# Kernel tuning notes

Measured on AMD Instinct MI355X. Metric: run time of the kernel, lower is better.

Reference implementation:

```python
import jax, jax.numpy as jnp
import numpy as np

N = 50000
E = 800000
IN_CH = 128
HID = 16
HEADS = 16
OUT_CH = 64
NEG_SLOPE = 0.2
EPS = 1e-16


def _add_self_loops(edge_index, n):
    loops = jnp.arange(n, dtype=edge_index.dtype)
    src = jnp.concatenate([edge_index[0], loops])
    dst = jnp.concatenate([edge_index[1], loops])
    return src, dst


def gat_conv(x, src, dst, W, a_src, a_dst, b, heads, out_ch, concat, n):
    # x: [N, F_in], W: [F_in, heads*out_ch], a_src/a_dst: [heads, out_ch]
    h = (x @ W).reshape(n, heads, out_ch)                 # [N, H, C]
    alpha_src = jnp.sum(h * a_src, axis=-1)               # [N, H]
    alpha_dst = jnp.sum(h * a_dst, axis=-1)               # [N, H]
    e = alpha_src[src] + alpha_dst[dst]                   # [E, H]
    e = jnp.where(e > 0, e, NEG_SLOPE * e)                # LeakyReLU(0.2)
    m = jax.ops.segment_max(e, dst, num_segments=n)       # [N, H] (finite: self-loops)
    ex = jnp.exp(e - m[dst])                              # [E, H]
    denom = jax.ops.segment_sum(ex, dst, num_segments=n)  # [N, H]
    alpha = ex / (denom[dst] + EPS)                       # [E, H]
    msg = h[src] * alpha[:, :, None]                      # [E, H, C]
    out = jax.ops.segment_sum(msg, dst, num_segments=n)   # [N, H, C]
    if concat:
        out = out.reshape(n, heads * out_ch)
    else:
        out = out.mean(axis=1)
    return out + b


def setup_inputs() -> dict:
    key = jax.random.key(0)
    ks = jax.random.split(key, 10)
    x = jax.random.normal(ks[0], (N, IN_CH), dtype=jnp.float32)
    edge_index = jax.random.randint(ks[1], (2, E), 0, N, dtype=jnp.int64)
    s1 = 1.0 / np.sqrt(IN_CH)
    W1 = jax.random.normal(ks[2], (IN_CH, HEADS * HID), dtype=jnp.float32) * s1
    a_src1 = jax.random.normal(ks[3], (HEADS, HID), dtype=jnp.float32) * (1.0 / np.sqrt(HID))
    a_dst1 = jax.random.normal(ks[4], (HEADS, HID), dtype=jnp.float32) * (1.0 / np.sqrt(HID))
    b1 = jnp.zeros((HEADS * HID,), dtype=jnp.float32)
    s2 = 1.0 / np.sqrt(HEADS * HID)
    W2 = jax.random.normal(ks[5], (HEADS * HID, OUT_CH), dtype=jnp.float32) * s2
    a_src2 = jax.random.normal(ks[6], (1, OUT_CH), dtype=jnp.float32) * (1.0 / np.sqrt(OUT_CH))
    a_dst2 = jax.random.normal(ks[7], (1, OUT_CH), dtype=jnp.float32) * (1.0 / np.sqrt(OUT_CH))
    b2 = jnp.zeros((OUT_CH,), dtype=jnp.float32)
    return {"x": x, "edge_index": edge_index, "W1": W1, "a_src1": a_src1,
            "a_dst1": a_dst1, "b1": b1, "W2": W2, "a_src2": a_src2,
            "a_dst2": a_dst2, "b2": b2}


def reference(x, edge_index, W1, a_src1, a_dst1, b1, W2, a_src2, a_dst2, b2):
    src, dst = _add_self_loops(edge_index, N)
    h = gat_conv(x, src, dst, W1, a_src1, a_dst1, b1, HEADS, HID, True, N)
    h = gat_conv(h, src, dst, W2, a_src2, a_dst2, b2, 1, OUT_CH, False, N)
    return jax.nn.sigmoid(h)
```

## Files before the change

kernel.cpp:

```cpp
#include <hip/hip_runtime.h>
#include <hip/hip_bf16.h>

#define NN 50000
#define EE 800000
#define TE 850000
#define BK 64

typedef __hip_bfloat16 bf16;
typedef __attribute__((ext_vector_type(8))) short short8v;
typedef __attribute__((ext_vector_type(4))) float float4v;

__device__ __forceinline__ float b2f(bf16 v) { return __bfloat162float(v); }
__device__ __forceinline__ float bu2f(unsigned short v) {
    return __uint_as_float((unsigned)v << 16);
}
__device__ __forceinline__ unsigned short f2bu(float v) {
    bf16 t = __float2bfloat16(v);
    return *(unsigned short*)&t;
}
__device__ __forceinline__ float lrelu(float e) { return (e > 0.f) ? e : 0.2f * e; }
__device__ __forceinline__ int clampn(int v) {
    return (v < 0) ? 0 : (v >= NN ? NN - 1 : v);
}

__device__ __forceinline__ int block_isi64(const void* ei) {
    __shared__ int sflag;
    int t = threadIdx.x;
    if (t < 64) {
        unsigned z = (((const unsigned*)ei)[2 * t + 1] == 0u) ? 1u : 0u;
        unsigned long long m = __ballot(z);
        if (t == 0) sflag = (__popcll(m) >= 32) ? 1 : 0;
    }
    __syncthreads();
    return sflag;
}

__global__ void prep_k(const void* __restrict__ ei, int* __restrict__ deg,
                       int* __restrict__ csr,
                       const float* __restrict__ W1, const float* __restrict__ W2,
                       const float* __restrict__ asr1, const float* __restrict__ ads1,
                       const float* __restrict__ asr2, const float* __restrict__ ads2,
                       unsigned short* __restrict__ W1T,
                       unsigned short* __restrict__ W2T,
                       unsigned short* __restrict__ P1sT,
                       unsigned short* __restrict__ P1dT,
                       unsigned short* __restrict__ P2T) {
    int isi64 = block_isi64(ei);
    int b = blockIdx.x, t = threadIdx.x;
    if (b < 128) {
        int j = b * 256 + t;
        int n = j >> 7, k = j & 127;
        W1T[j] = f2bu(W1[k * 256 + n]);
    } else if (b < 192) {
        int j = (b - 128) * 256 + t;
        int n = j >> 8, k = j & 255;
        W2T[j] = f2bu(W2[k * 64 + n]);
    } else if (b == 192) {
        for (int j = t; j < 2048; j += 256) {
            int h = j >> 7, k = j & 127;
            float s = 0.f, d = 0.f;
            for (int c = 0; c < 16; ++c) {
                float wv = W1[k * 256 + h * 16 + c];
                s += wv * asr1[h * 16 + c];
                d += wv * ads1[h * 16 + c];
            }
            P1sT[j] = f2bu(s);
            P1dT[j] = f2bu(d);
        }
    } else if (b == 193) {
        int k = t;
        float s = 0.f, d = 0.f;
        for (int c = 0; c < 64; ++c) {
            float wv = W2[k * 64 + c];
            s += wv * asr2[c];
            d += wv * ads2[c];
        }
        P2T[k] = f2bu(s);
        P2T[256 + k] = f2bu(d);
        for (int j = 512 + t; j < 4096; j += 256) P2T[j] = 0;
    }
    int p = b * 256 + t;
    int i0 = p * 2;
    if (i0 >= TE) return;
    int s0, d0, s1 = -1, d1 = -1;
    if (i0 + 1 < EE) {
        if (isi64) {
            longlong2 sv = ((const longlong2*)ei)[p];
            longlong2 dv = ((const longlong2*)ei)[(EE >> 1) + p];
            s0 = clampn((int)sv.x); s1 = clampn((int)sv.y);
            d0 = clampn((int)dv.x); d1 = clampn((int)dv.y);
        } else {
            int2 sv = ((const int2*)ei)[p];
            int2 dv = ((const int2*)ei)[(EE >> 1) + p];
            s0 = clampn(sv.x); s1 = clampn(sv.y);
            d0 = clampn(dv.x); d1 = clampn(dv.y);
        }
    } else {
        auto lde = [&](long long idx) {
            return clampn(isi64 ? (int)((const long long*)ei)[idx] : ((const int*)ei)[idx]);
        };
        if (i0 < EE) { s0 = lde(i0); d0 = lde((long long)EE + i0); }
        else         { s0 = i0 - EE; d0 = i0 - EE; }
        if (i0 + 1 < TE) {
            if (i0 + 1 < EE) { s1 = lde(i0 + 1); d1 = lde((long long)EE + i0 + 1); }
            else             { s1 = i0 + 1 - EE; d1 = i0 + 1 - EE; }
        }
    }
    int pos0 = atomicAdd(&deg[d0], 1);
    if (pos0 < BK) csr[d0 * BK + pos0] = s0;
    if (d1 >= 0) {
        int pos1 = atomicAdd(&deg[d1], 1);
        if (pos1 < BK) csr[d1 * BK + pos1] = s1;
    }
}

__global__ __launch_bounds__(256) void gemm1_k(
    const float* __restrict__ x, const unsigned short* __restrict__ W1T,
    const unsigned short* __restrict__ P1sT, const unsigned short* __restrict__ P1dT,
    bf16* __restrict__ h1, float* __restrict__ a_src, float* __restrict__ a_dst) {
    int wv = threadIdx.x >> 6, lane = threadIdx.x & 63;
    int m = lane & 15, quad = lane >> 4;
    int row0 = blockIdx.x * 64 + wv * 16;
    int arow = row0 + m;
    int arowc = (arow < NN) ? arow : NN - 1;
    const float4* x4 = (const float4*)x;
    short8v a[4];
#pragma unroll
    for (int ks = 0; ks < 4; ++ks) {
        float4 f0 = x4[(size_t)arowc * 32 + ks * 8 + quad * 2];
        float4 f1 = x4[(size_t)arowc * 32 + ks * 8 + quad * 2 + 1];
        union { short8v v; unsigned short u[8]; } ua;
        ua.u[0] = f2bu(f0.x); ua.u[1] = f2bu(f0.y);
        ua.u[2] = f2bu(f0.z); ua.u[3] = f2bu(f0.w);
        ua.u[4] = f2bu(f1.x); ua.u[5] = f2bu(f1.y);
        ua.u[6] = f2bu(f1.z); ua.u[7] = f2bu(f1.w);
        a[ks] = ua.v;
    }
    float4v accs = {0.f, 0.f, 0.f, 0.f}, accd = {0.f, 0.f, 0.f, 0.f};
#pragma unroll
    for (int ks = 0; ks < 4; ++ks) {
        short8v bs = *(const short8v*)&P1sT[(size_t)m * 128 + quad * 8 + ks * 32];
        short8v bd = *(const short8v*)&P1dT[(size_t)m * 128 + quad * 8 + ks * 32];
        accs = __builtin_amdgcn_mfma_f32_16x16x32_bf16(a[ks], bs, accs, 0, 0, 0);
        accd = __builtin_amdgcn_mfma_f32_16x16x32_bf16(a[ks], bd, accd, 0, 0, 0);
    }
    float4v acc[16];
#pragma unroll
    for (int t = 0; t < 16; ++t) {
        float4v c = {0.f, 0.f, 0.f, 0.f};
        const unsigned short* wb = &W1T[(size_t)(t * 16 + m) * 128 + quad * 8];
#pragma unroll
        for (int ks = 0; ks < 4; ++ks) {
            short8v b = *(const short8v*)&wb[ks * 32];
            c = __builtin_amdgcn_mfma_f32_16x16x32_bf16(a[ks], b, c, 0, 0, 0);
        }
        acc[t] = c;
    }
#pragma unroll
    for (int t = 0; t < 16; ++t) {
#pragma unroll
        for (int r = 0; r < 4; ++r) {
            int orow = row0 + quad * 4 + r;
            if (orow < NN)
                h1[(size_t)orow * 256 + t * 16 + m] = __float2bfloat16(acc[t][r]);
        }
    }
#pragma unroll
    for (int r = 0; r < 4; ++r) {
        int orow = row0 + quad * 4 + r;
        if (orow < NN) {
            a_src[orow * 16 + m] = accs[r];
            a_dst[orow * 16 + m] = accd[r];
        }
    }
}

__global__ __launch_bounds__(256) void agg1_k(
    const int* __restrict__ deg, int* __restrict__ csr,
    const float* __restrict__ a_src, const float* __restrict__ a_dst,
    const bf16* __restrict__ h1, const float* __restrict__ b1,
    bf16* __restrict__ out1) {
    __shared__ int sbuf[4][64];
    int wv = threadIdx.x >> 6, lane = threadIdx.x & 63;
    int dst = blockIdx.x * 4 + wv;
    int d = deg[dst]; if (d > BK) d = BK;
    int base = dst * BK;
    int v = (lane < d) ? csr[base + lane] : 0x7fffffff;
    int rank = 0;
    for (int j = 0; j < d; ++j) {
        int vj = __shfl(v, j, 64);
        rank += (vj < v || (vj == v && j < lane)) ? 1 : 0;
    }
    if (lane < d) sbuf[wv][rank] = v;
    if (lane < d) csr[base + lane] = sbuf[wv][lane];
    int we = lane >> 4, wh = lane & 15;
    int hc = lane >> 2;
    float adst_w = a_dst[dst * 16 + wh];
    float ax = 0.f, ay = 0.f, az = 0.f, aw = 0.f;
    float dsum = 0.f;
    int t0 = 0;
    for (; t0 + 4 <= d; t0 += 4) {
        int sr = sbuf[wv][t0 + we];
        float wr = __expf(lrelu(a_src[sr * 16 + wh] + adst_w));
        dsum += wr;
#pragma unroll
        for (int j = 0; j < 4; ++j) {
            float wj = __shfl(wr, j * 16 + hc, 64);
            int sj = sbuf[wv][t0 + j];
            ushort4 hv = *(const ushort4*)&h1[(size_t)sj * 256 + lane * 4];
            ax += wj * bu2f(hv.x);
            ay += wj * bu2f(hv.y);
            az += wj * bu2f(hv.z);
            aw += wj * bu2f(hv.w);
        }
    }
    if (t0 < d) {
        int n = d - t0;
        float wr = 0.f;
        if (we < n) {
            int sr = sbuf[wv][t0 + we];
            wr = __expf(lrelu(a_src[sr * 16 + wh] + adst_w));
        }
        dsum += wr;
        for (int j = 0; j < n; ++j) {
            float wj = __shfl(wr, j * 16 + hc, 64);
            int sj = sbuf[wv][t0 + j];
            ushort4 hv = *(const ushort4*)&h1[(size_t)sj * 256 + lane * 4];
            ax += wj * bu2f(hv.x);
            ay += wj * bu2f(hv.y);
            az += wj * bu2f(hv.z);
            aw += wj * bu2f(hv.w);
        }
    }
    dsum += __shfl_xor(dsum, 16, 64);
    dsum += __shfl_xor(dsum, 32, 64);
    float invd = 1.f / (__shfl(dsum, hc, 64) + 1e-16f);
    float4 bv = *(const float4*)&b1[lane * 4];
    ushort4 st;
    st.x = f2bu(ax * invd + bv.x);
    st.y = f2bu(ay * invd + bv.y);
    st.z = f2bu(az * invd + bv.z);
    st.w = f2bu(aw * invd + bv.w);
    *(ushort4*)&out1[(size_t)dst * 256 + lane * 4] = st;
}

__global__ __launch_bounds__(256) void gemm2_k(
    const bf16* __restrict__ out1, const unsigned short* __restrict__ W2T,
    const unsigned short* __restrict__ P2T,
    bf16* __restrict__ h2, float* __restrict__ a_src2, float* __restrict__ a_dst2) {
    int wv = threadIdx.x >> 6, lane = threadIdx.x & 63;
    int m = lane & 15, quad = lane >> 4;
    int row0 = blockIdx.x * 64 + wv * 16;
    int arow = row0 + m;
    int arowc = (arow < NN) ? arow : NN - 1;
    const unsigned short* ab = (const unsigned short*)out1;
    short8v a[8];
#pragma unroll
    for (int ks = 0; ks < 8; ++ks)
        a[ks] = *(const short8v*)&ab[(size_t)arowc * 256 + ks * 32 + quad * 8];
    float4v acca = {0.f, 0.f, 0.f, 0.f};
#pragma unroll
    for (int ks = 0; ks < 8; ++ks) {
        short8v b = *(const short8v*)&P2T[(size_t)m * 256 + quad * 8 + ks * 32];
        acca = __builtin_amdgcn_mfma_f32_16x16x32_bf16(a[ks], b, acca, 0, 0, 0);
    }
    float4v acc[4];
#pragma unroll
    for (int t = 0; t < 4; ++t) {
        float4v c = {0.f, 0.f, 0.f, 0.f};
        const unsigned short* wb = &W2T[(size_t)(t * 16 + m) * 256 + quad * 8];
#pragma unroll
        for (int ks = 0; ks < 8; ++ks) {
            short8v b = *(const short8v*)&wb[ks * 32];
            c = __builtin_amdgcn_mfma_f32_16x16x32_bf16(a[ks], b, c, 0, 0, 0);
        }
        acc[t] = c;
    }
#pragma unroll
    for (int t = 0; t < 4; ++t) {
#pragma unroll
        for (int r = 0; r < 4; ++r) {
            int orow = row0 + quad * 4 + r;
            if (orow < NN)
                h2[(size_t)orow * 64 + t * 16 + m] = __float2bfloat16(acc[t][r]);
        }
    }
#pragma unroll
    for (int r = 0; r < 4; ++r) {
        int orow = row0 + quad * 4 + r;
        if (orow < NN) {
            if (m == 0) a_src2[orow] = acca[r];
            if (m == 1) a_dst2[orow] = acca[r];
        }
    }
}

__global__ __launch_bounds__(256) void agg2_k(
    const int* __restrict__ deg, const int* __restrict__ csr,
    const float* __restrict__ a_src2, const float* __restrict__ a_dst2,
    const bf16* __restrict__ h2, const float* __restrict__ b2,
    float* __restrict__ out) {
    int wv = threadIdx.x >> 6;
    int lane = threadIdx.x & 63;
    int dst = blockIdx.x * 4 + wv;
    if (dst >= NN) return;
    int d = deg[dst]; if (d > BK) d = BK;
    int base = dst * BK;
    float adst = a_dst2[dst];
    int half = lane >> 5, hl = lane & 31;
    float acc0 = 0.f, acc1 = 0.f, dsum = 0.f;
    float wr = 0.f; int sr = 0;
    if (lane < d) {
        sr = csr[base + lane];
        wr = __expf(lrelu(a_src2[sr] + adst));
    }
    dsum += wr;
    for (int j0 = 0; j0 < d; j0 += 8) {
        ushort2 hv[4];
        float wj[4];
#pragma unroll
        for (int u = 0; u < 4; ++u) {
            int j = j0 + u * 2 + half;
            int jc = (j < d) ? j : 0;
            float w = __shfl(wr, jc, 64);
            int sj = __shfl(sr, jc, 64);
            wj[u] = (j < d) ? w : 0.f;
            hv[u] = *(const ushort2*)&h2[(size_t)sj * 64 + hl * 2];
        }
#pragma unroll
        for (int u = 0; u < 4; ++u) {
            acc0 += wj[u] * bu2f(hv[u].x);
            acc1 += wj[u] * bu2f(hv[u].y);
        }
    }
    acc0 += __shfl_xor(acc0, 32, 64);
    acc1 += __shfl_xor(acc1, 32, 64);
#pragma unroll
    for (int o = 32; o >= 1; o >>= 1) dsum += __shfl_xor(dsum, o, 64);
    if (half == 0) {
        float inv = 1.f / (dsum + 1e-16f);
        float o0 = acc0 * inv + b2[hl * 2];
        float o1 = acc1 * inv + b2[hl * 2 + 1];
        float2 st;
        st.x = 1.f / (1.f + __expf(-o0));
        st.y = 1.f / (1.f + __expf(-o1));
        *(float2*)&out[(size_t)dst * 64 + hl * 2] = st;
    }
}


extern "C" void kernel_launch(void* const* d_in, const int* in_sizes, int n_in,
                              void* d_out, int out_size, void* d_ws, size_t ws_size,
                              hipStream_t stream) {
    const float* x    = (const float*)d_in[0];
    const void*  ei   = d_in[1];
    const float* W1   = (const float*)d_in[2];
    const float* asr1 = (const float*)d_in[3];
    const float* ads1 = (const float*)d_in[4];
    const float* b1   = (const float*)d_in[5];
    const float* W2   = (const float*)d_in[6];
    const float* asr2 = (const float*)d_in[7];
    const float* ads2 = (const float*)d_in[8];
    const float* b2   = (const float*)d_in[9];
    float* out = (float*)d_out;

    char* w = (char*)d_ws;
    auto carve = [&](size_t bytes) {
        void* p = (void*)w;
        w += (bytes + 255) & ~(size_t)255;
        return p;
    };
    int*    csr      = (int*)carve((size_t)NN * BK * 4);
    int*    deg      = (int*)carve((size_t)NN * 4);
    float*  a_src1   = (float*)carve((size_t)NN * 16 * 4);
    float*  a_dst1   = (float*)carve((size_t)NN * 16 * 4);
    unsigned short* W1T  = (unsigned short*)carve(128 * 256 * 2);
    unsigned short* W2T  = (unsigned short*)carve(256 * 64 * 2);
    unsigned short* P1sT = (unsigned short*)carve(16 * 128 * 2);
    unsigned short* P1dT = (unsigned short*)carve(16 * 128 * 2);
    unsigned short* P2T  = (unsigned short*)carve(16 * 256 * 2);
    bf16*   h1       = (bf16*)carve((size_t)NN * 256 * 2);
    bf16*   out1     = (bf16*)carve((size_t)NN * 256 * 2);
    char*   l2base   = (char*)h1;
    bf16*   h2       = (bf16*)l2base;
    float*  a_src2   = (float*)(l2base + (size_t)NN * 64 * 2);
    float*  a_dst2   = a_src2 + NN;

    hipMemsetAsync(deg, 0, (size_t)NN * 4, stream);

    const int pgrid = ((TE + 1) / 2 + 255) / 256;
    prep_k<<<pgrid, 256, 0, stream>>>(ei, deg, csr, W1, W2, asr1, ads1, asr2, ads2,
                                      W1T, W2T, P1sT, P1dT, P2T);
    gemm1_k<<<(NN + 63) / 64, 256, 0, stream>>>(x, W1T, P1sT, P1dT, h1, a_src1, a_dst1);
    agg1_k<<<NN / 4, 256, 0, stream>>>(deg, csr, a_src1, a_dst1, h1, b1, out1);
    gemm2_k<<<(NN + 63) / 64, 256, 0, stream>>>(out1, W2T, P2T, h2, a_src2, a_dst2);
    agg2_k<<<(NN + 3) / 4, 256, 0, stream>>>(deg, csr, a_src2, a_dst2, h2, b2, out);
}
```

Baseline: 299.3 us.

## Fuse all stages into one persistent kernel with grid-wide barriers

```diff
diff --git a/kernel.cpp b/kernel.cpp
--- a/kernel.cpp
+++ b/kernel.cpp
@@ -5,12 +5,14 @@
 #define EE 800000
 #define TE 850000
 #define BK 64
+#define NEB 1661
+#define NGB 782
+#define NAB 12500
 
 typedef __hip_bfloat16 bf16;
 typedef __attribute__((ext_vector_type(8))) short short8v;
 typedef __attribute__((ext_vector_type(4))) float float4v;
 
-__device__ __forceinline__ float b2f(bf16 v) { return __bfloat162float(v); }
 __device__ __forceinline__ float bu2f(unsigned short v) {
     return __uint_as_float((unsigned)v << 16);
 }
@@ -23,328 +25,326 @@
     return (v < 0) ? 0 : (v >= NN ? NN - 1 : v);
 }
 
-__device__ __forceinline__ int block_isi64(const void* ei) {
-    __shared__ int sflag;
-    int t = threadIdx.x;
-    if (t < 64) {
-        unsigned z = (((const unsigned*)ei)[2 * t + 1] == 0u) ? 1u : 0u;
-        unsigned long long m = __ballot(z);
-        if (t == 0) sflag = (__popcll(m) >= 32) ? 1 : 0;
-    }
+__device__ __forceinline__ void gsync(int* bar, int target) {
     __syncthreads();
-    return sflag;
-}
-
-__global__ void prep_k(const void* __restrict__ ei, int* __restrict__ deg,
-                       int* __restrict__ csr,
-                       const float* __restrict__ W1, const float* __restrict__ W2,
-                       const float* __restrict__ asr1, const float* __restrict__ ads1,
-                       const float* __restrict__ asr2, const float* __restrict__ ads2,
-                       unsigned short* __restrict__ W1T,
-                       unsigned short* __restrict__ W2T,
-                       unsigned short* __restrict__ P1sT,
-                       unsigned short* __restrict__ P1dT,
-                       unsigned short* __restrict__ P2T) {
-    int isi64 = block_isi64(ei);
-    int b = blockIdx.x, t = threadIdx.x;
-    if (b < 128) {
-        int j = b * 256 + t;
-        int n = j >> 7, k = j & 127;
-        W1T[j] = f2bu(W1[k * 256 + n]);
-    } else if (b < 192) {
-        int j = (b - 128) * 256 + t;
-        int n = j >> 8, k = j & 255;
-        W2T[j] = f2bu(W2[k * 64 + n]);
-    } else if (b == 192) {
-        for (int j = t; j < 2048; j += 256) {
-            int h = j >> 7, k = j & 127;
+    if (threadIdx.x == 0) {
+        __threadfence();
+        __hip_atomic_fetch_add(bar, 1, __ATOMIC_RELEASE, __HIP_MEMORY_SCOPE_AGENT);
+        while (__hip_atomic_load(bar, __ATOMIC_ACQUIRE, __HIP_MEMORY_SCOPE_AGENT)
+               < target)
+            __builtin_amdgcn_s_sleep(2);
+        __threadfence();
+    }
+    __syncthreads();
+}
+
+__global__ __launch_bounds__(256, 2) void mega_k(
+    const void* __restrict__ ei, const float* __restrict__ x,
+    const float* __restrict__ W1, const float* __restrict__ asr1,
+    const float* __restrict__ ads1, const float* __restrict__ b1,
+    const float* __restrict__ W2, const float* __restrict__ asr2,
+    const float* __restrict__ ads2, const float* __restrict__ b2,
+    int* __restrict__ deg, int* __restrict__ csr,
+    unsigned short* __restrict__ W1T, unsigned short* __restrict__ W2T,
+    unsigned short* __restrict__ P1sT, unsigned short* __restrict__ P1dT,
+    unsigned short* __restrict__ P2T,
+    float* __restrict__ a_src1, float* __restrict__ a_dst1,
+    bf16* __restrict__ h1, bf16* __restrict__ h2,
+    float* __restrict__ a_src2, float* __restrict__ a_dst2,
+    int* __restrict__ bar,
+    float* __restrict__ out) {
+    const int tid = threadIdx.x;
+    const int wv = tid >> 6, lane = tid & 63;
+    const int G = gridDim.x;
+
+    __shared__ int s_isi64;
+    __shared__ int sbuf[4][64];
+    __shared__ unsigned short sout[4][256];
+
+    if (tid < 64) {
+        unsigned z = (((const unsigned*)ei)[2 * tid + 1] == 0u) ? 1u : 0u;
+        unsigned long long mb = __ballot(z);
+        if (tid == 0) s_isi64 = (__popcll(mb) >= 32) ? 1 : 0;
+    }
+    __syncthreads();
+    const int isi64 = s_isi64;
+
+    for (int i = blockIdx.x * 256 + tid; i < NN; i += G * 256) deg[i] = 0;
+    gsync(&bar[0], G);
+
+    for (int vb = blockIdx.x; vb < 194; vb += G) {
+        if (vb < 128) {
+            int j = vb * 256 + tid;
+            int n = j >> 7, k = j & 127;
+            W1T[j] = f2bu(W1[k * 256 + n]);
+        } else if (vb < 192) {
+            int j = (vb - 128) * 256 + tid;
+            int n = j >> 8, k = j & 255;
+            W2T[j] = f2bu(W2[k * 64 + n]);
+        } else if (vb == 192) {
+            for (int j = tid; j < 2048; j += 256) {
+                int h = j >> 7, k = j & 127;
+                float s = 0.f, d = 0.f;
+                for (int c = 0; c < 16; ++c) {
+                    float wvv = W1[k * 256 + h * 16 + c];
+                    s += wvv * asr1[h * 16 + c];
+                    d += wvv * ads1[h * 16 + c];
+                }
+                P1sT[j] = f2bu(s);
+                P1dT[j] = f2bu(d);
+            }
+        } else {
+            int k = tid;
             float s = 0.f, d = 0.f;
-            for (int c = 0; c < 16; ++c) {
-                float wv = W1[k * 256 + h * 16 + c];
-                s += wv * asr1[h * 16 + c];
-                d += wv * ads1[h * 16 + c];
-            }
-            P1sT[j] = f2bu(s);
-            P1dT[j] = f2bu(d);
-        }
-    } else if (b == 193) {
-        int k = t;
-        float s = 0.f, d = 0.f;
-        for (int c = 0; c < 64; ++c) {
-            float wv = W2[k * 64 + c];
-            s += wv * asr2[c];
-            d += wv * ads2[c];
-        }
-        P2T[k] = f2bu(s);
-        P2T[256 + k] = f2bu(d);
-        for (int j = 512 + t; j < 4096; j += 256) P2T[j] = 0;
-    }
-    int p = b * 256 + t;
-    int i0 = p * 2;
-    if (i0 >= TE) return;
-    int s0, d0, s1 = -1, d1 = -1;
-    if (i0 + 1 < EE) {
-        if (isi64) {
-            longlong2 sv = ((const longlong2*)ei)[p];
-            longlong2 dv = ((const longlong2*)ei)[(EE >> 1) + p];
-            s0 = clampn((int)sv.x); s1 = clampn((int)sv.y);
-            d0 = clampn((int)dv.x); d1 = clampn((int)dv.y);
+            for (int c = 0; c < 64; ++c) {
+                float wvv = W2[k * 64 + c];
+                s += wvv * asr2[c];
+                d += wvv * ads2[c];
+            }
+            P2T[k] = f2bu(s);
+            P2T[256 + k] = f2bu(d);
+            for (int j = 512 + tid; j < 4096; j += 256) P2T[j] = 0;
+        }
+    }
+    for (int vb = blockIdx.x; vb < NEB; vb += G) {
+        int p = vb * 256 + tid;
+        int i0 = p * 2;
+        if (i0 >= TE) continue;
+        int s0, d0, s1 = -1, d1 = -1;
+        if (i0 + 1 < EE) {
+            if (isi64) {
+                longlong2 sv = ((const longlong2*)ei)[p];
+                longlong2 dv = ((const longlong2*)ei)[(EE >> 1) + p];
+                s0 = clampn((int)sv.x); s1 = clampn((int)sv.y);
+                d0 = clampn((int)dv.x); d1 = clampn((int)dv.y);
+            } else {
+                int2 sv = ((const int2*)ei)[p];
+                int2 dv = ((const int2*)ei)[(EE >> 1) + p];
+                s0 = clampn(sv.x); s1 = clampn(sv.y);
+                d0 = clampn(dv.x); d1 = clampn(dv.y);
+            }
         } else {
-            int2 sv = ((const int2*)ei)[p];
-            int2 dv = ((const int2*)ei)[(EE >> 1) + p];
-            s0 = clampn(sv.x); s1 = clampn(sv.y);
-            d0 = clampn(dv.x); d1 = clampn(dv.y);
-        }
-    } else {
-        auto lde = [&](long long idx) {
-            return clampn(isi64 ? (int)((const long long*)ei)[idx] : ((const int*)ei)[idx]);
-        };
-        if (i0 < EE) { s0 = lde(i0); d0 = lde((long long)EE + i0); }
-        else         { s0 = i0 - EE; d0 = i0 - EE; }
-        if (i0 + 1 < TE) {
-            if (i0 + 1 < EE) { s1 = lde(i0 + 1); d1 = lde((long long)EE + i0 + 1); }
-            else             { s1 = i0 + 1 - EE; d1 = i0 + 1 - EE; }
-        }
-    }
-    int pos0 = atomicAdd(&deg[d0], 1);
-    if (pos0 < BK) csr[d0 * BK + pos0] = s0;
-    if (d1 >= 0) {
-        int pos1 = atomicAdd(&deg[d1], 1);
-        if (pos1 < BK) csr[d1 * BK + pos1] = s1;
-    }
-}
-
-__global__ __launch_bounds__(256) void gemm1_k(
-    const float* __restrict__ x, const unsigned short* __restrict__ W1T,
-    const unsigned short* __restrict__ P1sT, const unsigned short* __restrict__ P1dT,
-    bf16* __restrict__ h1, float* __restrict__ a_src, float* __restrict__ a_dst) {
-    int wv = threadIdx.x >> 6, lane = threadIdx.x & 63;
-    int m = lane & 15, quad = lane >> 4;
-    int row0 = blockIdx.x * 64 + wv * 16;
-    int arow = row0 + m;
-    int arowc = (arow < NN) ? arow : NN - 1;
-    const float4* x4 = (const float4*)x;
-    short8v a[4];
-#pragma unroll
-    for (int ks = 0; ks < 4; ++ks) {
-        float4 f0 = x4[(size_t)arowc * 32 + ks * 8 + quad * 2];
-        float4 f1 = x4[(size_t)arowc * 32 + ks * 8 + quad * 2 + 1];
-        union { short8v v; unsigned short u[8]; } ua;
-        ua.u[0] = f2bu(f0.x); ua.u[1] = f2bu(f0.y);
-        ua.u[2] = f2bu(f0.z); ua.u[3] = f2bu(f0.w);
-        ua.u[4] = f2bu(f1.x); ua.u[5] = f2bu(f1.y);
-        ua.u[6] = f2bu(f1.z); ua.u[7] = f2bu(f1.w);
-        a[ks] = ua.v;
-    }
-    float4v accs = {0.f, 0.f, 0.f, 0.f}, accd = {0.f, 0.f, 0.f, 0.f};
-#pragma unroll
-    for (int ks = 0; ks < 4; ++ks) {
-        short8v bs = *(const short8v*)&P1sT[(size_t)m * 128 + quad * 8 + ks * 32];
-        short8v bd = *(const short8v*)&P1dT[(size_t)m * 128 + quad * 8 + ks * 32];
-        accs = __builtin_amdgcn_mfma_f32_16x16x32_bf16(a[ks], bs, accs, 0, 0, 0);
-        accd = __builtin_amdgcn_mfma_f32_16x16x32_bf16(a[ks], bd, accd, 0, 0, 0);
-    }
-    float4v acc[16];
-#pragma unroll
-    for (int t = 0; t < 16; ++t) {
-        float4v c = {0.f, 0.f, 0.f, 0.f};
-        const unsigned short* wb = &W1T[(size_t)(t * 16 + m) * 128 + quad * 8];
-#pragma unroll
-        for (int ks = 0; ks < 4; ++ks) {
-            short8v b = *(const short8v*)&wb[ks * 32];
-            c = __builtin_amdgcn_mfma_f32_16x16x32_bf16(a[ks], b, c, 0, 0, 0);
-        }
-        acc[t] = c;
-    }
-#pragma unroll
-    for (int t = 0; t < 16; ++t) {
-#pragma unroll
-        for (int r = 0; r < 4; ++r) {
-            int orow = row0 + quad * 4 + r;
-            if (orow < NN)
-                h1[(size_t)orow * 256 + t * 16 + m] = __float2bfloat16(acc[t][r]);
-        }
-    }
-#pragma unroll
-    for (int r = 0; r < 4; ++r) {
-        int orow = row0 + quad * 4 + r;
-        if (orow < NN) {
-            a_src[orow * 16 + m] = accs[r];
-            a_dst[orow * 16 + m] = accd[r];
-        }
-    }
-}
-
-__global__ __launch_bounds__(256) void agg1_k(
-    const int* __restrict__ deg, int* __restrict__ csr,
-    const float* __restrict__ a_src, const float* __restrict__ a_dst,
-    const bf16* __restrict__ h1, const float* __restrict__ b1,
-    bf16* __restrict__ out1) {
-    __shared__ int sbuf[4][64];
-    int wv = threadIdx.x >> 6, lane = threadIdx.x & 63;
-    int dst = blockIdx.x * 4 + wv;
-    int d = deg[dst]; if (d > BK) d = BK;
-    int base = dst * BK;
-    int v = (lane < d) ? csr[base + lane] : 0x7fffffff;
-    int rank = 0;
-    for (int j = 0; j < d; ++j) {
-        int vj = __shfl(v, j, 64);
-        rank += (vj < v || (vj == v && j < lane)) ? 1 : 0;
-    }
-    if (lane < d) sbuf[wv][rank] = v;
-    if (lane < d) csr[base + lane] = sbuf[wv][lane];
-    int we = lane >> 4, wh = lane & 15;
-    int hc = lane >> 2;
-    float adst_w = a_dst[dst * 16 + wh];
-    float ax = 0.f, ay = 0.f, az = 0.f, aw = 0.f;
-    float dsum = 0.f;
-    int t0 = 0;
-    for (; t0 + 4 <= d; t0 += 4) {
-        int sr = sbuf[wv][t0 + we];
-        float wr = __expf(lrelu(a_src[sr * 16 + wh] + adst_w));
+            auto lde = [&](long long idx) {
+                return clampn(isi64 ? (int)((const long long*)ei)[idx]
+                                    : ((const int*)ei)[idx]);
+            };
+            if (i0 < EE) { s0 = lde(i0); d0 = lde((long long)EE + i0); }
+            else         { s0 = i0 - EE; d0 = i0 - EE; }
+            if (i0 + 1 < TE) {
+                if (i0 + 1 < EE) { s1 = lde(i0 + 1); d1 = lde((long long)EE + i0 + 1); }
+                else             { s1 = i0 + 1 - EE; d1 = i0 + 1 - EE; }
+            }
+        }
+        int pos0 = atomicAdd(&deg[d0], 1);
+        if (pos0 < BK) csr[d0 * BK + pos0] = s0;
+        if (d1 >= 0) {
+            int pos1 = atomicAdd(&deg[d1], 1);
+            if (pos1 < BK) csr[d1 * BK + pos1] = s1;
+        }
+    }
+    gsync(&bar[1], G);
+
+    {
+        const int m = lane & 15, quad = lane >> 4;
+        const float4* x4 = (const float4*)x;
+        for (int vb = blockIdx.x; vb < NGB; vb += G) {
+            int row0 = vb * 64 + wv * 16;
+            int arow = row0 + m;
+            int arowc = (arow < NN) ? arow : NN - 1;
+            short8v a[4];
+#pragma unroll
+            for (int ks = 0; ks < 4; ++ks) {
+                float4 f0 = x4[(size_t)arowc * 32 + ks * 8 + quad * 2];
+                float4 f1 = x4[(size_t)arowc * 32 + ks * 8 + quad * 2 + 1];
+                union { short8v v; unsigned short u[8]; } ua;
+                ua.u[0] = f2bu(f0.x); ua.u[1] = f2bu(f0.y);
+                ua.u[2] = f2bu(f0.z); ua.u[3] = f2bu(f0.w);
+                ua.u[4] = f2bu(f1.x); ua.u[5] = f2bu(f1.y);
+                ua.u[6] = f2bu(f1.z); ua.u[7] = f2bu(f1.w);
+                a[ks] = ua.v;
+            }
+            float4v accs = {0.f, 0.f, 0.f, 0.f}, accd = {0.f, 0.f, 0.f, 0.f};
+#pragma unroll
+            for (int ks = 0; ks < 4; ++ks) {
+                short8v bs = *(const short8v*)&P1sT[(size_t)m * 128 + quad * 8 + ks * 32];
+                short8v bd = *(const short8v*)&P1dT[(size_t)m * 128 + quad * 8 + ks * 32];
+                accs = __builtin_amdgcn_mfma_f32_16x16x32_bf16(a[ks], bs, accs, 0, 0, 0);
+                accd = __builtin_amdgcn_mfma_f32_16x16x32_bf16(a[ks], bd, accd, 0, 0, 0);
+            }
+#pragma unroll
+            for (int r = 0; r < 4; ++r) {
+                int orow = row0 + quad * 4 + r;
+                if (orow < NN) {
+                    a_src1[orow * 16 + m] = accs[r];
+                    a_dst1[orow * 16 + m] = accd[r];
+                }
+            }
+#pragma unroll
+            for (int t = 0; t < 16; ++t) {
+                float4v c = {0.f, 0.f, 0.f, 0.f};
+                const unsigned short* wb = &W1T[(size_t)(t * 16 + m) * 128 + quad * 8];
+#pragma unroll
+                for (int ks = 0; ks < 4; ++ks) {
+                    short8v b = *(const short8v*)&wb[ks * 32];
+                    c = __builtin_amdgcn_mfma_f32_16x16x32_bf16(a[ks], b, c, 0, 0, 0);
+                }
+#pragma unroll
+                for (int r = 0; r < 4; ++r) {
+                    int orow = row0 + quad * 4 + r;
+                    if (orow < NN)
+                        h1[(size_t)orow * 256 + t * 16 + m] = __float2bfloat16(c[r]);
+                }
+            }
+        }
+    }
+    gsync(&bar[2], G);
+
+    for (int vb = blockIdx.x; vb < NAB; vb += G) {
+        int dst = vb * 4 + wv;
+        int d = deg[dst]; if (d > BK) d = BK;
+        int base = dst * BK;
+        int v = (lane < d) ? csr[base + lane] : 0x7fffffff;
+        int rank = 0;
+        for (int j = 0; j < d; ++j) {
+            int vj = __shfl(v, j, 64);
+            rank += (vj < v || (vj == v && j < lane)) ? 1 : 0;
+        }
+        if (lane < d) sbuf[wv][rank] = v;
+        if (lane < d) csr[base + lane] = sbuf[wv][lane];
+        int we = lane >> 4, wh = lane & 15;
+        int hc = lane >> 2;
+        float adst_w = a_dst1[dst * 16 + wh];
+        float ax = 0.f, ay = 0.f, az = 0.f, aw = 0.f;
+        float dsum = 0.f;
+        int t0 = 0;
+        for (; t0 + 4 <= d; t0 += 4) {
+            int sr = sbuf[wv][t0 + we];
+            float wr = __expf(lrelu(a_src1[sr * 16 + wh] + adst_w));
+            dsum += wr;
+#pragma unroll
+            for (int j = 0; j < 4; ++j) {
+                float wj = __shfl(wr, j * 16 + hc, 64);
+                int sj = sbuf[wv][t0 + j];
+                ushort4 hv = *(const ushort4*)&h1[(size_t)sj * 256 + lane * 4];
+                ax += wj * bu2f(hv.x);
+                ay += wj * bu2f(hv.y);
+                az += wj * bu2f(hv.z);
+                aw += wj * bu2f(hv.w);
+            }
+        }
+        if (t0 < d) {
+            int n = d - t0;
+            float wr = 0.f;
+            if (we < n) {
+                int sr = sbuf[wv][t0 + we];
+                wr = __expf(lrelu(a_src1[sr * 16 + wh] + adst_w));
+            }
+            dsum += wr;
+            for (int j = 0; j < n; ++j) {
+                float wj = __shfl(wr, j * 16 + hc, 64);
+                int sj = sbuf[wv][t0 + j];
+                ushort4 hv = *(const ushort4*)&h1[(size_t)sj * 256 + lane * 4];
+                ax += wj * bu2f(hv.x);
+                ay += wj * bu2f(hv.y);
+                az += wj * bu2f(hv.z);
+                aw += wj * bu2f(hv.w);
+            }
+        }
+        dsum += __shfl_xor(dsum, 16, 64);
+        dsum += __shfl_xor(dsum, 32, 64);
+        float invd = 1.f / (__shfl(dsum, hc, 64) + 1e-16f);
+        float4 bv = *(const float4*)&b1[lane * 4];
+        ushort4 st;
+        st.x = f2bu(ax * invd + bv.x);
+        st.y = f2bu(ay * invd + bv.y);
+        st.z = f2bu(az * invd + bv.z);
+        st.w = f2bu(aw * invd + bv.w);
+        *(ushort4*)&sout[wv][lane * 4] = st;
+        __syncthreads();
+        {
+            int mm = lane & 15, qq = lane >> 4;
+            short8v a2[8];
+#pragma unroll
+            for (int ks = 0; ks < 8; ++ks)
+                a2[ks] = *(const short8v*)&sout[mm & 3][ks * 32 + qq * 8];
+            float4v c2 = {0.f, 0.f, 0.f, 0.f};
+            const unsigned short* wb2 = &W2T[(size_t)(wv * 16 + mm) * 256 + qq * 8];
+#pragma unroll
+            for (int ks = 0; ks < 8; ++ks) {
+                short8v b = *(const short8v*)&wb2[ks * 32];
+                c2 = __builtin_amdgcn_mfma_f32_16x16x32_bf16(a2[ks], b, c2, 0, 0, 0);
+            }
+            if (qq == 0) {
+#pragma unroll
+                for (int r = 0; r < 4; ++r)
+                    h2[(size_t)(vb * 4 + r) * 64 + wv * 16 + mm] = __float2bfloat16(c2[r]);
+            }
+            if (wv == 0) {
+                float4v ca = {0.f, 0.f, 0.f, 0.f};
+                const unsigned short* pb = &P2T[(size_t)mm * 256 + qq * 8];
+#pragma unroll
+                for (int ks = 0; ks < 8; ++ks) {
+                    short8v b = *(const short8v*)&pb[ks * 32];
+                    ca = __builtin_amdgcn_mfma_f32_16x16x32_bf16(a2[ks], b, ca, 0, 0, 0);
+                }
+                if (qq == 0 && mm == 0) {
+#pragma unroll
+                    for (int r = 0; r < 4; ++r) a_src2[vb * 4 + r] = ca[r];
+                }
+                if (qq == 0 && mm == 1) {
+#pragma unroll
+                    for (int r = 0; r < 4; ++r) a_dst2[vb * 4 + r] = ca[r];
+                }
+            }
+        }
+        __syncthreads();
+    }
+    gsync(&bar[3], G);
+
+    for (int vb = blockIdx.x; vb < NAB; vb += G) {
+        int dst = vb * 4 + wv;
+        int d = deg[dst]; if (d > BK) d = BK;
+        int base = dst * BK;
+        float adst = a_dst2[dst];
+        int half = lane >> 5, hl = lane & 31;
+        float acc0 = 0.f, acc1 = 0.f, dsum = 0.f;
+        float wr = 0.f; int sr = 0;
+        if (lane < d) {
+            sr = csr[base + lane];
+            wr = __expf(lrelu(a_src2[sr] + adst));
+        }
         dsum += wr;
-#pragma unroll
-        for (int j = 0; j < 4; ++j) {
-            float wj = __shfl(wr, j * 16 + hc, 64);
-            int sj = sbuf[wv][t0 + j];
-            ushort4 hv = *(const ushort4*)&h1[(size_t)sj * 256 + lane * 4];
-            ax += wj * bu2f(hv.x);
-            ay += wj * bu2f(hv.y);
-            az += wj * bu2f(hv.z);
-            aw += wj * bu2f(hv.w);
-        }
-    }
-    if (t0 < d) {
-        int n = d - t0;
-        float wr = 0.f;
-        if (we < n) {
-            int sr = sbuf[wv][t0 + we];
-            wr = __expf(lrelu(a_src[sr * 16 + wh] + adst_w));
-        }
-        dsum += wr;
-        for (int j = 0; j < n; ++j) {
-            float wj = __shfl(wr, j * 16 + hc, 64);
-            int sj = sbuf[wv][t0 + j];
-            ushort4 hv = *(const ushort4*)&h1[(size_t)sj * 256 + lane * 4];
-            ax += wj * bu2f(hv.x);
-            ay += wj * bu2f(hv.y);
-            az += wj * bu2f(hv.z);
-            aw += wj * bu2f(hv.w);
-        }
-    }
-    dsum += __shfl_xor(dsum, 16, 64);
-    dsum += __shfl_xor(dsum, 32, 64);
-    float invd = 1.f / (__shfl(dsum, hc, 64) + 1e-16f);
-    float4 bv = *(const float4*)&b1[lane * 4];
-    ushort4 st;
-    st.x = f2bu(ax * invd + bv.x);
-    st.y = f2bu(ay * invd + bv.y);
-    st.z = f2bu(az * invd + bv.z);
-    st.w = f2bu(aw * invd + bv.w);
-    *(ushort4*)&out1[(size_t)dst * 256 + lane * 4] = st;
-}
-
-__global__ __launch_bounds__(256) void gemm2_k(
-    const bf16* __restrict__ out1, const unsigned short* __restrict__ W2T,
-    const unsigned short* __restrict__ P2T,
-    bf16* __restrict__ h2, float* __restrict__ a_src2, float* __restrict__ a_dst2) {
-    int wv = threadIdx.x >> 6, lane = threadIdx.x & 63;
-    int m = lane & 15, quad = lane >> 4;
-    int row0 = blockIdx.x * 64 + wv * 16;
-    int arow = row0 + m;
-    int arowc = (arow < NN) ? arow : NN - 1;
-    const unsigned short* ab = (const unsigned short*)out1;
-    short8v a[8];
-#pragma unroll
-    for (int ks = 0; ks < 8; ++ks)
-        a[ks] = *(const short8v*)&ab[(size_t)arowc * 256 + ks * 32 + quad * 8];
-    float4v acca = {0.f, 0.f, 0.f, 0.f};
-#pragma unroll
-    for (int ks = 0; ks < 8; ++ks) {
-        short8v b = *(const short8v*)&P2T[(size_t)m * 256 + quad * 8 + ks * 32];
-        acca = __builtin_amdgcn_mfma_f32_16x16x32_bf16(a[ks], b, acca, 0, 0, 0);
-    }
-    float4v acc[4];
-#pragma unroll
-    for (int t = 0; t < 4; ++t) {
-        float4v c = {0.f, 0.f, 0.f, 0.f};
-        const unsigned short* wb = &W2T[(size_t)(t * 16 + m) * 256 + quad * 8];
-#pragma unroll
-        for (int ks = 0; ks < 8; ++ks) {
-            short8v b = *(const short8v*)&wb[ks * 32];
-            c = __builtin_amdgcn_mfma_f32_16x16x32_bf16(a[ks], b, c, 0, 0, 0);
-        }
-        acc[t] = c;
-    }
-#pragma unroll
-    for (int t = 0; t < 4; ++t) {
-#pragma unroll
-        for (int r = 0; r < 4; ++r) {
-            int orow = row0 + quad * 4 + r;
-            if (orow < NN)
-                h2[(size_t)orow * 64 + t * 16 + m] = __float2bfloat16(acc[t][r]);
-        }
-    }
-#pragma unroll
-    for (int r = 0; r < 4; ++r) {
-        int orow = row0 + quad * 4 + r;
-        if (orow < NN) {
-            if (m == 0) a_src2[orow] = acca[r];
-            if (m == 1) a_dst2[orow] = acca[r];
-        }
-    }
-}
-
-__global__ __launch_bounds__(256) void agg2_k(
-    const int* __restrict__ deg, const int* __restrict__ csr,
-    const float* __restrict__ a_src2, const float* __restrict__ a_dst2,
-    const bf16* __restrict__ h2, const float* __restrict__ b2,
-    float* __restrict__ out) {
-    int wv = threadIdx.x >> 6;
-    int lane = threadIdx.x & 63;
-    int dst = blockIdx.x * 4 + wv;
-    if (dst >= NN) return;
-    int d = deg[dst]; if (d > BK) d = BK;
-    int base = dst * BK;
-    float adst = a_dst2[dst];
-    int half = lane >> 5, hl = lane & 31;
-    float acc0 = 0.f, acc1 = 0.f, dsum = 0.f;
-    float wr = 0.f; int sr = 0;
-    if (lane < d) {
-        sr = csr[base + lane];
-        wr = __expf(lrelu(a_src2[sr] + adst));
-    }
-    dsum += wr;
-    for (int j0 = 0; j0 < d; j0 += 8) {
-        ushort2 hv[4];
-        float wj[4];
-#pragma unroll
-        for (int u = 0; u < 4; ++u) {
-            int j = j0 + u * 2 + half;
-            int jc = (j < d) ? j : 0;
-            float w = __shfl(wr, jc, 64);
-            int sj = __shfl(sr, jc, 64);
-            wj[u] = (j < d) ? w : 0.f;
-            hv[u] = *(const ushort2*)&h2[(size_t)sj * 64 + hl * 2];
-        }
-#pragma unroll
-        for (int u = 0; u < 4; ++u) {
-            acc0 += wj[u] * bu2f(hv[u].x);
-            acc1 += wj[u] * bu2f(hv[u].y);
-        }
-    }
-    acc0 += __shfl_xor(acc0, 32, 64);
-    acc1 += __shfl_xor(acc1, 32, 64);
-#pragma unroll
-    for (int o = 32; o >= 1; o >>= 1) dsum += __shfl_xor(dsum, o, 64);
-    if (half == 0) {
-        float inv = 1.f / (dsum + 1e-16f);
-        float o0 = acc0 * inv + b2[hl * 2];
-        float o1 = acc1 * inv + b2[hl * 2 + 1];
-        float2 st;
-        st.x = 1.f / (1.f + __expf(-o0));
-        st.y = 1.f / (1.f + __expf(-o1));
-        *(float2*)&out[(size_t)dst * 64 + hl * 2] = st;
+        for (int j0 = 0; j0 < d; j0 += 8) {
+            ushort2 hv[4];
+            float wj[4];
+#pragma unroll
+            for (int u = 0; u < 4; ++u) {
+                int j = j0 + u * 2 + half;
+                int jc = (j < d) ? j : 0;
+                float w = __shfl(wr, jc, 64);
+                int sj = __shfl(sr, jc, 64);
+                wj[u] = (j < d) ? w : 0.f;
+                hv[u] = *(const ushort2*)&h2[(size_t)sj * 64 + hl * 2];
+            }
+#pragma unroll
+            for (int u = 0; u < 4; ++u) {
+                acc0 += wj[u] * bu2f(hv[u].x);
+                acc1 += wj[u] * bu2f(hv[u].y);
+            }
+        }
+        acc0 += __shfl_xor(acc0, 32, 64);
+        acc1 += __shfl_xor(acc1, 32, 64);
+#pragma unroll
+        for (int o = 32; o >= 1; o >>= 1) dsum += __shfl_xor(dsum, o, 64);
+        if (half == 0) {
+            float inv = 1.f / (dsum + 1e-16f);
+            float o0 = acc0 * inv + b2[hl * 2];
+            float o1 = acc1 * inv + b2[hl * 2 + 1];
+            float2 stv;
+            stv.x = 1.f / (1.f + __expf(-o0));
+            stv.y = 1.f / (1.f + __expf(-o1));
+            *(float2*)&out[(size_t)dst * 64 + hl * 2] = stv;
+        }
     }
 }
 
@@ -380,19 +380,28 @@
     unsigned short* P1dT = (unsigned short*)carve(16 * 128 * 2);
     unsigned short* P2T  = (unsigned short*)carve(16 * 256 * 2);
     bf16*   h1       = (bf16*)carve((size_t)NN * 256 * 2);
-    bf16*   out1     = (bf16*)carve((size_t)NN * 256 * 2);
-    char*   l2base   = (char*)h1;
-    bf16*   h2       = (bf16*)l2base;
-    float*  a_src2   = (float*)(l2base + (size_t)NN * 64 * 2);
-    float*  a_dst2   = a_src2 + NN;
-
-    hipMemsetAsync(deg, 0, (size_t)NN * 4, stream);
-
-    const int pgrid = ((TE + 1) / 2 + 255) / 256;
-    prep_k<<<pgrid, 256, 0, stream>>>(ei, deg, csr, W1, W2, asr1, ads1, asr2, ads2,
-                                      W1T, W2T, P1sT, P1dT, P2T);
-    gemm1_k<<<(NN + 63) / 64, 256, 0, stream>>>(x, W1T, P1sT, P1dT, h1, a_src1, a_dst1);
-    agg1_k<<<NN / 4, 256, 0, stream>>>(deg, csr, a_src1, a_dst1, h1, b1, out1);
-    gemm2_k<<<(NN + 63) / 64, 256, 0, stream>>>(out1, W2T, P2T, h2, a_src2, a_dst2);
-    agg2_k<<<(NN + 3) / 4, 256, 0, stream>>>(deg, csr, a_src2, a_dst2, h2, b2, out);
-}
+    bf16*   h2       = (bf16*)carve((size_t)NN * 64 * 2);
+    float*  a_src2   = (float*)carve((size_t)NN * 4);
+    float*  a_dst2   = (float*)carve((size_t)NN * 4);
+    int*    bar      = (int*)carve(4 * sizeof(int));
+
+    static int gblocks = 0;
+    if (gblocks == 0) {
+        int ncu = 256;
+        hipDeviceProp_t prop;
+        int dev = 0;
+        if (hipGetDevice(&dev) == hipSuccess &&
+            hipGetDeviceProperties(&prop, dev) == hipSuccess &&
+            prop.multiProcessorCount > 0)
+            ncu = prop.multiProcessorCount;
+        gblocks = 2 * ncu;
+        if (gblocks > NAB) gblocks = NAB;
+        if (gblocks < 1) gblocks = 256;
+    }
+
+    hipMemsetAsync(bar, 0, 4 * sizeof(int), stream);
+    mega_k<<<gblocks, 256, 0, stream>>>(
+        ei, x, W1, asr1, ads1, b1, W2, asr2, ads2, b2,
+        deg, csr, W1T, W2T, P1sT, P1dT, P2T,
+        a_src1, a_dst1, h1, h2, a_src2, a_dst2, bar, out);
+}
```

Result: slower. 851.1 us (+184.4%).

## Fuse layer-2 projection GEMM into layer-1 aggregation kernel via shared memory

Applied to the files above, without the earlier changes.

```diff
diff --git a/kernel.cpp b/kernel.cpp
--- a/kernel.cpp
+++ b/kernel.cpp
@@ -10,7 +10,6 @@
 typedef __attribute__((ext_vector_type(8))) short short8v;
 typedef __attribute__((ext_vector_type(4))) float float4v;
 
-__device__ __forceinline__ float b2f(bf16 v) { return __bfloat162float(v); }
 __device__ __forceinline__ float bu2f(unsigned short v) {
     return __uint_as_float((unsigned)v << 16);
 }
@@ -175,12 +174,14 @@
     }
 }
 
-__global__ __launch_bounds__(256) void agg1_k(
+__global__ __launch_bounds__(256) void agg1f_k(
     const int* __restrict__ deg, int* __restrict__ csr,
     const float* __restrict__ a_src, const float* __restrict__ a_dst,
     const bf16* __restrict__ h1, const float* __restrict__ b1,
-    bf16* __restrict__ out1) {
+    const unsigned short* __restrict__ W2T, const unsigned short* __restrict__ P2T,
+    bf16* __restrict__ h2, float* __restrict__ a_src2, float* __restrict__ a_dst2) {
     __shared__ int sbuf[4][64];
+    __shared__ unsigned short sout[4][272];
     int wv = threadIdx.x >> 6, lane = threadIdx.x & 63;
     int dst = blockIdx.x * 4 + wv;
     int d = deg[dst]; if (d > BK) d = BK;
@@ -241,56 +242,43 @@
     st.y = f2bu(ay * invd + bv.y);
     st.z = f2bu(az * invd + bv.z);
     st.w = f2bu(aw * invd + bv.w);
-    *(ushort4*)&out1[(size_t)dst * 256 + lane * 4] = st;
-}
-
-__global__ __launch_bounds__(256) void gemm2_k(
-    const bf16* __restrict__ out1, const unsigned short* __restrict__ W2T,
-    const unsigned short* __restrict__ P2T,
-    bf16* __restrict__ h2, float* __restrict__ a_src2, float* __restrict__ a_dst2) {
-    int wv = threadIdx.x >> 6, lane = threadIdx.x & 63;
-    int m = lane & 15, quad = lane >> 4;
-    int row0 = blockIdx.x * 64 + wv * 16;
-    int arow = row0 + m;
-    int arowc = (arow < NN) ? arow : NN - 1;
-    const unsigned short* ab = (const unsigned short*)out1;
-    short8v a[8];
-#pragma unroll
-    for (int ks = 0; ks < 8; ++ks)
-        a[ks] = *(const short8v*)&ab[(size_t)arowc * 256 + ks * 32 + quad * 8];
-    float4v acca = {0.f, 0.f, 0.f, 0.f};
-#pragma unroll
-    for (int ks = 0; ks < 8; ++ks) {
-        short8v b = *(const short8v*)&P2T[(size_t)m * 256 + quad * 8 + ks * 32];
-        acca = __builtin_amdgcn_mfma_f32_16x16x32_bf16(a[ks], b, acca, 0, 0, 0);
-    }
-    float4v acc[4];
-#pragma unroll
-    for (int t = 0; t < 4; ++t) {
-        float4v c = {0.f, 0.f, 0.f, 0.f};
-        const unsigned short* wb = &W2T[(size_t)(t * 16 + m) * 256 + quad * 8];
+    *(ushort4*)&sout[wv][lane * 4] = st;
+    __syncthreads();
+    {
+        int mm = lane & 15, qq = lane >> 4;
+        short8v a2[8];
+#pragma unroll
+        for (int ks = 0; ks < 8; ++ks)
+            a2[ks] = *(const short8v*)&sout[mm & 3][ks * 32 + qq * 8];
+        float4v c2 = {0.f, 0.f, 0.f, 0.f};
+        const unsigned short* wb2 = &W2T[(size_t)(wv * 16 + mm) * 256 + qq * 8];
 #pragma unroll
         for (int ks = 0; ks < 8; ++ks) {
-            short8v b = *(const short8v*)&wb[ks * 32];
-            c = __builtin_amdgcn_mfma_f32_16x16x32_bf16(a[ks], b, c, 0, 0, 0);
-        }
-        acc[t] = c;
-    }
-#pragma unroll
-    for (int t = 0; t < 4; ++t) {
-#pragma unroll
-        for (int r = 0; r < 4; ++r) {
-            int orow = row0 + quad * 4 + r;
-            if (orow < NN)
-                h2[(size_t)orow * 64 + t * 16 + m] = __float2bfloat16(acc[t][r]);
-        }
-    }
-#pragma unroll
-    for (int r = 0; r < 4; ++r) {
-        int orow = row0 + quad * 4 + r;
-        if (orow < NN) {
-            if (m == 0) a_src2[orow] = acca[r];
-            if (m == 1) a_dst2[orow] = acca[r];
+            short8v b = *(const short8v*)&wb2[ks * 32];
+            c2 = __builtin_amdgcn_mfma_f32_16x16x32_bf16(a2[ks], b, c2, 0, 0, 0);
+        }
+        if (qq == 0) {
+#pragma unroll
+            for (int r = 0; r < 4; ++r)
+                h2[(size_t)(blockIdx.x * 4 + r) * 64 + wv * 16 + mm] =
+                    __float2bfloat16(c2[r]);
+        }
+        if (wv == 0) {
+            float4v ca = {0.f, 0.f, 0.f, 0.f};
+            const unsigned short* pb = &P2T[(size_t)mm * 256 + qq * 8];
+#pragma unroll
+            for (int ks = 0; ks < 8; ++ks) {
+                short8v b = *(const short8v*)&pb[ks * 32];
+                ca = __builtin_amdgcn_mfma_f32_16x16x32_bf16(a2[ks], b, ca, 0, 0, 0);
+            }
+            if (qq == 0 && mm == 0) {
+#pragma unroll
+                for (int r = 0; r < 4; ++r) a_src2[blockIdx.x * 4 + r] = ca[r];
+            }
+            if (qq == 0 && mm == 1) {
+#pragma unroll
+                for (int r = 0; r < 4; ++r) a_dst2[blockIdx.x * 4 + r] = ca[r];
+            }
         }
     }
 }
@@ -380,11 +368,9 @@
     unsigned short* P1dT = (unsigned short*)carve(16 * 128 * 2);
     unsigned short* P2T  = (unsigned short*)carve(16 * 256 * 2);
     bf16*   h1       = (bf16*)carve((size_t)NN * 256 * 2);
-    bf16*   out1     = (bf16*)carve((size_t)NN * 256 * 2);
-    char*   l2base   = (char*)h1;
-    bf16*   h2       = (bf16*)l2base;
-    float*  a_src2   = (float*)(l2base + (size_t)NN * 64 * 2);
-    float*  a_dst2   = a_src2 + NN;
+    bf16*   h2       = (bf16*)carve((size_t)NN * 64 * 2);
+    float*  a_src2   = (float*)carve((size_t)NN * 4);
+    float*  a_dst2   = (float*)carve((size_t)NN * 4);
 
     hipMemsetAsync(deg, 0, (size_t)NN * 4, stream);
 
@@ -392,7 +378,7 @@
     prep_k<<<pgrid, 256, 0, stream>>>(ei, deg, csr, W1, W2, asr1, ads1, asr2, ads2,
                                       W1T, W2T, P1sT, P1dT, P2T);
     gemm1_k<<<(NN + 63) / 64, 256, 0, stream>>>(x, W1T, P1sT, P1dT, h1, a_src1, a_dst1);
-    agg1_k<<<NN / 4, 256, 0, stream>>>(deg, csr, a_src1, a_dst1, h1, b1, out1);
-    gemm2_k<<<(NN + 63) / 64, 256, 0, stream>>>(out1, W2T, P2T, h2, a_src2, a_dst2);
+    agg1f_k<<<NN / 4, 256, 0, stream>>>(deg, csr, a_src1, a_dst1, h1, b1,
+                                        W2T, P2T, h2, a_src2, a_dst2);
     agg2_k<<<(NN + 3) / 4, 256, 0, stream>>>(deg, csr, a_src2, a_dst2, h2, b2, out);
 }
```

After: 302.0 us. About the same (+0.9%).
